# Optimization experiments

Measured on AMD Instinct MI355X. Metric: run time of the kernel, lower is better.

Reference implementation:

```python
import jax, jax.numpy as jnp
import numpy as np

N_HEAD = 12
D_MODEL = 768


def setup_inputs() -> dict:
    key = jax.random.key(0)
    ks = jax.random.split(key, 5)
    B, S, D = 8, 1024, D_MODEL
    return {
        "x": jax.random.normal(ks[0], (B, S, D), dtype=jnp.float32),
        "Wqkv": jax.random.normal(ks[1], (D, 3 * D), dtype=jnp.float32) * 0.02,
        "bqkv": jax.random.normal(ks[2], (3 * D,), dtype=jnp.float32) * 0.02,
        "Wproj": jax.random.normal(ks[3], (D, D), dtype=jnp.float32) * 0.02,
        "bproj": jax.random.normal(ks[4], (D,), dtype=jnp.float32) * 0.02,
    }


def _attention(x, Wqkv, bqkv, Wproj, bproj):
    B, S, D = x.shape
    hd = D // N_HEAD
    qkv = x @ Wqkv + bqkv                      # [B,S,3D]
    q, k, v = jnp.split(qkv, 3, axis=-1)
    # split heads -> [B,H,S,hd]
    def sh(t):
        return t.reshape(B, S, N_HEAD, hd).transpose(0, 2, 1, 3)
    q, k, v = sh(q), sh(k), sh(v)
    scores = jnp.einsum("bhqd,bhkd->bhqk", q, k) / jnp.sqrt(jnp.float32(hd))
    causal = jnp.tril(jnp.ones((S, S), dtype=bool))  # [S,S]
    mask_value = jnp.finfo(scores.dtype).min
    scores = jnp.where(causal[None, None], scores, mask_value)
    attn = jax.nn.softmax(scores, axis=-1)
    # dropout p=0.1 treated as identity (eval mode)
    out = jnp.einsum("bhqk,bhkd->bhqd", attn, v)
    out = out.transpose(0, 2, 1, 3).reshape(B, S, D)  # merge heads
    return out @ Wproj + bproj


def reference(x, Wqkv, bqkv, Wproj, bproj):
    return _attention(x, Wqkv, bqkv, Wproj, bproj)
```

## Files before the change

kernel.cpp:

```cpp
#include <hip/hip_runtime.h>
#include <cstddef>

typedef float f32x4 __attribute__((ext_vector_type(4)));
typedef short s16x4 __attribute__((ext_vector_type(4)));
typedef short s16x8 __attribute__((ext_vector_type(8)));
typedef __bf16 bf16x8 __attribute__((ext_vector_type(8)));

#define NB 8
#define NS 1024
#define ND 768
#define NH 12
#define HD 64

__device__ __forceinline__ unsigned short f2bf(float f) {
  unsigned u = __builtin_bit_cast(unsigned, f);
  u += 0x7fffu + ((u >> 16) & 1u);
  return (unsigned short)(u >> 16);
}

__device__ __forceinline__ f32x4 mfma16(bf16x8 a, bf16x8 b, f32x4 c) {
  return __builtin_amdgcn_mfma_f32_16x16x32_bf16(a, b, c, 0, 0, 0);
}

__device__ __forceinline__ bf16x8 ld8(const unsigned short* p) {
  return *reinterpret_cast<const bf16x8*>(p);
}

__device__ __forceinline__ void gload16(unsigned short* lds_dst, const unsigned short* gsrc) {
  __builtin_amdgcn_global_load_lds(
      (const __attribute__((address_space(1))) unsigned int*)gsrc,
      (__attribute__((address_space(3))) unsigned int*)lds_dst, 16, 0, 0);
}

#define VMW(N) asm volatile("s_waitcnt vmcnt(" #N ")" ::: "memory")


__global__ __launch_bounds__(256) void cvt_f32_bf16(const float* __restrict__ in,
                                                    unsigned short* __restrict__ out) {
  int i = (blockIdx.x * 256 + threadIdx.x) * 4;
  float4 v = *reinterpret_cast<const float4*>(in + i);
  ushort4 o;
  o.x = f2bf(v.x); o.y = f2bf(v.y); o.z = f2bf(v.z); o.w = f2bf(v.w);
  *reinterpret_cast<ushort4*>(out + i) = o;
}

__global__ __launch_bounds__(256) void transpose_cvt(const float* __restrict__ in,
                                                     unsigned short* __restrict__ out,
                                                     int R, int C) {
  __shared__ float tile[32][33];
  int c0 = blockIdx.x * 32, r0 = blockIdx.y * 32;
  int tx = threadIdx.x & 31, ty = threadIdx.x >> 5;
#pragma unroll
  for (int i = 0; i < 32; i += 8)
    tile[ty + i][tx] = in[(size_t)(r0 + ty + i) * C + c0 + tx];
  __syncthreads();
#pragma unroll
  for (int i = 0; i < 32; i += 8)
    out[(size_t)(c0 + ty + i) * R + r0 + tx] = f2bf(tile[tx][ty + i]);
}


#define SLOT 8192

__device__ __forceinline__ void gemm_mainloop4(const unsigned short* __restrict__ A,
                                               const unsigned short* __restrict__ Bt,
                                               int K, int m0, int n0,
                                               unsigned short* smem,
                                               f32x4 (&acc)[4][4]) {
  int tid = threadIdx.x, lane = tid & 63, wid = tid >> 6;
  int wr = wid >> 1, wc = wid & 1;
  int ll = lane & 15, lh = lane >> 4;
  int swsrc = ((lane & 3) ^ ((lane >> 3) & 3)) * 8;

  const unsigned short* asrc = A + (size_t)(m0 + wid * 32 + (lane >> 2)) * K + swsrc;
  const unsigned short* bsrc = Bt + (size_t)(n0 + wid * 32 + (lane >> 2)) * K + swsrc;
  const int sw = (lh ^ ((ll >> 1) & 3)) * 8;
  const int nt = K / 32;

  auto stage = [&](int slot, int t) {
    unsigned short* ad = smem + slot * SLOT + wid * 1024;
    unsigned short* bd = smem + slot * SLOT + 4096 + wid * 1024;
    const unsigned short* as = asrc + t * 32;
    const unsigned short* bs = bsrc + t * 32;
    gload16(ad, as);
    gload16(ad + 512, as + (size_t)16 * K);
    gload16(bd, bs);
    gload16(bd + 512, bs + (size_t)16 * K);
  };

  stage(0, 0);
  stage(1, 1);
  stage(2, 2);
  VMW(8);
  __builtin_amdgcn_s_barrier();
  asm volatile("" ::: "memory");

  for (int t = 0; t < nt; ++t) {
    if (t + 3 < nt) stage((t + 3) & 3, t + 3);

    const unsigned short* Ab = smem + (t & 3) * SLOT;
    const unsigned short* Bb = Ab + 4096;

    __builtin_amdgcn_s_setprio(1);
    bf16x8 af[4], bg[4];
#pragma unroll
    for (int m = 0; m < 4; m++) af[m] = ld8(Ab + (wr * 64 + m * 16 + ll) * 32 + sw);
#pragma unroll
    for (int n = 0; n < 4; n++) bg[n] = ld8(Bb + (wc * 64 + n * 16 + ll) * 32 + sw);
#pragma unroll
    for (int m = 0; m < 4; m++)
#pragma unroll
      for (int n = 0; n < 4; n++) acc[m][n] = mfma16(af[m], bg[n], acc[m][n]);
    __builtin_amdgcn_s_setprio(0);

    if (t + 3 < nt) {
      VMW(8);
      __builtin_amdgcn_s_barrier();
      asm volatile("" ::: "memory");
    } else if (t + 2 < nt) {
      VMW(4);
      __builtin_amdgcn_s_barrier();
      asm volatile("" ::: "memory");
    } else if (t + 1 < nt) {
      VMW(0);
      __builtin_amdgcn_s_barrier();
      asm volatile("" ::: "memory");
    }
  }
}

__device__ __forceinline__ void gemm_mainloop3(const unsigned short* __restrict__ A,
                                               const unsigned short* __restrict__ Bt,
                                               int K, int m0, int n0,
                                               unsigned short* smem,
                                               f32x4 (&acc)[4][4]) {
  int tid = threadIdx.x, lane = tid & 63, wid = tid >> 6;
  int wr = wid >> 1, wc = wid & 1;
  int ll = lane & 15, lh = lane >> 4;
  int swsrc = ((lane & 3) ^ ((lane >> 3) & 3)) * 8;

  const unsigned short* asrc = A + (size_t)(m0 + wid * 32 + (lane >> 2)) * K + swsrc;
  const unsigned short* bsrc = Bt + (size_t)(n0 + wid * 32 + (lane >> 2)) * K + swsrc;
  const int sw = (lh ^ ((ll >> 1) & 3)) * 8;
  const int nt = K / 32;

  auto stage = [&](int slot, int t) {
    unsigned short* ad = smem + slot * SLOT + wid * 1024;
    unsigned short* bd = smem + slot * SLOT + 4096 + wid * 1024;
    const unsigned short* as = asrc + t * 32;
    const unsigned short* bs = bsrc + t * 32;
    gload16(ad, as);
    gload16(ad + 512, as + (size_t)16 * K);
    gload16(bd, bs);
    gload16(bd + 512, bs + (size_t)16 * K);
  };

  stage(0, 0);
  stage(1, 1);
  VMW(4);
  __builtin_amdgcn_s_barrier();
  asm volatile("" ::: "memory");

  int slot = 0;
  for (int t = 0; t < nt; ++t) {
    if (t + 2 < nt) {
      int s2 = slot + 2; if (s2 >= 3) s2 -= 3;
      stage(s2, t + 2);
    }
    const unsigned short* Ab = smem + slot * SLOT;
    const unsigned short* Bb = Ab + 4096;

    __builtin_amdgcn_s_setprio(1);
    bf16x8 af[4], bg[4];
#pragma unroll
    for (int m = 0; m < 4; m++) af[m] = ld8(Ab + (wr * 64 + m * 16 + ll) * 32 + sw);
#pragma unroll
    for (int n = 0; n < 4; n++) bg[n] = ld8(Bb + (wc * 64 + n * 16 + ll) * 32 + sw);
#pragma unroll
    for (int m = 0; m < 4; m++)
#pragma unroll
      for (int n = 0; n < 4; n++) acc[m][n] = mfma16(af[m], bg[n], acc[m][n]);
    __builtin_amdgcn_s_setprio(0);

    if (t + 2 < nt) {
      VMW(4);
      __builtin_amdgcn_s_barrier();
      asm volatile("" ::: "memory");
    } else if (t + 2 == nt) {
      VMW(0);
      __builtin_amdgcn_s_barrier();
      asm volatile("" ::: "memory");
    }
    slot++; if (slot == 3) slot = 0;
  }
}


#define QSCALE 0.18033688f

__global__ __launch_bounds__(256, 2) void qkv_gemm(const unsigned short* __restrict__ xbf,
                                                   const unsigned short* __restrict__ WT,
                                                   const float* __restrict__ bias,
                                                   unsigned short* __restrict__ qw,
                                                   unsigned short* __restrict__ kw,
                                                   unsigned short* __restrict__ vt) {
  __shared__ __align__(16) unsigned short smem[4 * SLOT];
  int bid = blockIdx.x;
  int k8 = bid & 7, j = bid >> 3;
  int m0 = (k8 * 8 + (j & 7)) * 128;
  int n0 = (j >> 3) * 128;
  f32x4 acc[4][4];
#pragma unroll
  for (int m = 0; m < 4; m++)
#pragma unroll
    for (int n = 0; n < 4; n++) acc[m][n] = (f32x4){0.f, 0.f, 0.f, 0.f};

  gemm_mainloop4(xbf, WT, ND, m0, n0, smem, acc);

  int tid = threadIdx.x, lane = tid & 63, wid = tid >> 6;
  int wr = wid >> 1, wc = wid & 1;
  int ll = lane & 15, lh = lane >> 4;
  int which = n0 / ND;

  if (which == 2) {
#pragma unroll
    for (int nf = 0; nf < 4; nf++) {
      int col = n0 + wc * 64 + nf * 16 + ll;
      float bv = bias[col];
      int w2 = col - 2 * ND;
      int h = w2 >> 6, d = w2 & 63;
#pragma unroll
      for (int mf = 0; mf < 4; mf++) {
        int m = m0 + wr * 64 + mf * 16 + lh * 4;
        int b = m >> 10, s = m & 1023;
        s16x4 pk;
        pk[0] = (short)f2bf(acc[mf][nf][0] + bv);
        pk[1] = (short)f2bf(acc[mf][nf][1] + bv);
        pk[2] = (short)f2bf(acc[mf][nf][2] + bv);
        pk[3] = (short)f2bf(acc[mf][nf][3] + bv);
        size_t idx = (((size_t)b * NH + h) * HD + d) * NS + s;
        *(s16x4*)&vt[idx] = pk;
      }
    }
  } else {
#pragma unroll
    for (int nf = 0; nf < 4; nf++) {
      int col = n0 + wc * 64 + nf * 16 + ll;
      float bv = bias[col];
      int w2 = col - which * ND;
      int h = w2 >> 6, d = w2 & 63;
#pragma unroll
      for (int mf = 0; mf < 4; mf++) {
#pragma unroll
        for (int r = 0; r < 4; r++) {
          int m = m0 + wr * 64 + mf * 16 + lh * 4 + r;
          int b = m >> 10, s = m & 1023;
          float v = acc[mf][nf][r] + bv;
          size_t idx = (((size_t)b * NH + h) * NS + s) * HD + d;
          if (which == 0)
            qw[idx] = f2bf(v * QSCALE);
          else
            kw[idx] = f2bf(v);
        }
      }
    }
  }
}


__global__ __launch_bounds__(256, 3) void proj_gemm(const unsigned short* __restrict__ abf,
                                                    const unsigned short* __restrict__ WT,
                                                    const float* __restrict__ bias,
                                                    float* __restrict__ out) {
  __shared__ __align__(16) unsigned short smem[3 * SLOT];
  int bid = blockIdx.x;
  int k8 = bid & 7, j = bid >> 3;
  int m0 = (k8 * 8 + (j & 7)) * 128;
  int n0 = (j >> 3) * 128;
  f32x4 acc[4][4];
#pragma unroll
  for (int m = 0; m < 4; m++)
#pragma unroll
    for (int n = 0; n < 4; n++) acc[m][n] = (f32x4){0.f, 0.f, 0.f, 0.f};

  gemm_mainloop3(abf, WT, ND, m0, n0, smem, acc);

  int tid = threadIdx.x, lane = tid & 63, wid = tid >> 6;
  int wr = wid >> 1, wc = wid & 1;
  int ll = lane & 15, lh = lane >> 4;
#pragma unroll
  for (int nf = 0; nf < 4; nf++) {
    int col = n0 + wc * 64 + nf * 16 + ll;
    float bv = bias[col];
#pragma unroll
    for (int mf = 0; mf < 4; mf++) {
#pragma unroll
      for (int r = 0; r < 4; r++) {
        int m = m0 + wr * 64 + mf * 16 + lh * 4 + r;
        out[(size_t)m * ND + col] = acc[mf][nf][r] + bv;
      }
    }
  }
}


#define LP 88
#define KVSLOT 8192

__global__ __launch_bounds__(512) void attn_kernel(const unsigned short* __restrict__ qw,
                                                   const unsigned short* __restrict__ kw,
                                                   const unsigned short* __restrict__ vt,
                                                   unsigned short* __restrict__ attn_out) {
  int bid = blockIdx.x;
  int xcd = bid & 7, j = bid >> 3;
  int grp = xcd * 12 + (j % 12);
  int qt = 7 - (j / 12);
  int b = grp / NH, h = grp % NH;
  __shared__ __align__(16) unsigned short KV[3 * KVSLOT];
  __shared__ __align__(16) unsigned short Ps[8][16 * LP];

  int tid = threadIdx.x, lane = tid & 63, wid = tid >> 6;
  int ll = lane & 15, lh = lane >> 4, r7x = ll & 7;
  int q0 = qt * 128, q0w = q0 + wid * 16;
  const size_t bhk = ((size_t)b * NH + h) * NS * HD;
  const size_t bhv = ((size_t)b * NH + h) * HD * NS;

  bf16x8 qf0 = ld8(&qw[bhk + (size_t)(q0w + ll) * HD + lh * 8]);
  bf16x8 qf1 = ld8(&qw[bhk + (size_t)(q0w + ll) * HD + 32 + lh * 8]);

  f32x4 o[4];
#pragma unroll
  for (int n = 0; n < 4; n++) o[n] = (f32x4){0.f, 0.f, 0.f, 0.f};
  float m_r = -1e30f, l_r = 0.f;

  int srow = tid >> 3;
  int scol = ((tid & 7) ^ ((tid >> 3) & 7)) * 8;
  const unsigned short* ksrc = kw + bhk + (size_t)srow * HD + scol;
  const unsigned short* vsrc = vt + bhv + (size_t)srow * NS + scol;

  unsigned short* pw = &Ps[wid][ll * LP];
  const int qme = q0w + ll;
  const int qmaxw = q0w + 15;
  const int nt = 2 * (qt + 1);

  auto stage = [&](int slot, int t) {
    unsigned short* kd = KV + slot * KVSLOT + wid * 512;
    unsigned short* vd = KV + slot * KVSLOT + 4096 + wid * 512;
    gload16(kd, ksrc + (size_t)t * 64 * HD);
    gload16(vd, vsrc + t * 64);
  };

  stage(0, 0);
  stage(1, 1);
  VMW(2);
  __builtin_amdgcn_s_barrier();
  asm volatile("" ::: "memory");

  int slot = 0;
  for (int t = 0; t < nt; ++t) {
    if (t + 2 < nt) {
      int s2 = slot + 2; if (s2 >= 3) s2 -= 3;
      stage(s2, t + 2);
    }
    int j0 = t * 64;

    if (j0 <= qmaxw) {
      const unsigned short* Kb = KV + slot * KVSLOT;
      const unsigned short* Vb = Kb + 4096;

      f32x4 sa[4];
#pragma unroll
      for (int n = 0; n < 4; n++) {
        bf16x8 kf0 = ld8(Kb + (n * 16 + ll) * 64 + (lh ^ r7x) * 8);
        bf16x8 kf1 = ld8(Kb + (n * 16 + ll) * 64 + ((4 + lh) ^ r7x) * 8);
        sa[n] = mfma16(kf0, qf0, (f32x4){0.f, 0.f, 0.f, 0.f});
        sa[n] = mfma16(kf1, qf1, sa[n]);
      }

      if (j0 + 63 > q0w) {
#pragma unroll
        for (int n = 0; n < 4; n++)
#pragma unroll
          for (int r = 0; r < 4; r++)
            if (j0 + n * 16 + lh * 4 + r > qme) sa[n][r] = -1e30f;
      }

      float t0 = fmaxf(fmaxf(sa[0][0], sa[0][1]), fmaxf(sa[0][2], sa[0][3]));
      float t1 = fmaxf(fmaxf(sa[1][0], sa[1][1]), fmaxf(sa[1][2], sa[1][3]));
      float t2 = fmaxf(fmaxf(sa[2][0], sa[2][1]), fmaxf(sa[2][2], sa[2][3]));
      float t3 = fmaxf(fmaxf(sa[3][0], sa[3][1]), fmaxf(sa[3][2], sa[3][3]));
      float tmax = fmaxf(fmaxf(t0, t1), fmaxf(t2, t3));
      tmax = fmaxf(tmax, __shfl_xor(tmax, 16));
      tmax = fmaxf(tmax, __shfl_xor(tmax, 32));

      if (!__all(tmax - m_r <= 11.5f)) {
        float mnew = fmaxf(m_r, tmax);
        float alpha = exp2f(m_r - mnew);
        m_r = mnew;
        l_r *= alpha;
        float ab0 = __shfl(alpha, lh * 4 + 0);
        float ab1 = __shfl(alpha, lh * 4 + 1);
        float ab2 = __shfl(alpha, lh * 4 + 2);
        float ab3 = __shfl(alpha, lh * 4 + 3);
#pragma unroll
        for (int n2 = 0; n2 < 4; n2++) {
          o[n2][0] *= ab0; o[n2][1] *= ab1; o[n2][2] *= ab2; o[n2][3] *= ab3;
        }
      }

      float p[4][4];
      float ssum = 0.f;
#pragma unroll
      for (int n = 0; n < 4; n++)
#pragma unroll
        for (int r = 0; r < 4; r++) {
          p[n][r] = exp2f(sa[n][r] - m_r);
          ssum += p[n][r];
        }
      ssum += __shfl_xor(ssum, 16);
      ssum += __shfl_xor(ssum, 32);
      l_r += ssum;

#pragma unroll
      for (int n = 0; n < 4; n++) {
        s16x4 pk;
        pk[0] = (short)f2bf(p[n][0]);
        pk[1] = (short)f2bf(p[n][1]);
        pk[2] = (short)f2bf(p[n][2]);
        pk[3] = (short)f2bf(p[n][3]);
        *(s16x4*)&pw[n * 16 + lh * 4] = pk;
      }

#pragma unroll
      for (int c = 0; c < 2; c++) {
        bf16x8 pf = ld8(&pw[c * 32 + lh * 8]);
#pragma unroll
        for (int n2 = 0; n2 < 4; n2++) {
          bf16x8 vf = ld8(Vb + (n2 * 16 + ll) * 64 + ((c * 4 + lh) ^ r7x) * 8);
          o[n2] = mfma16(pf, vf, o[n2]);
        }
      }
    }

    if (t + 2 < nt) {
      VMW(2);
      __builtin_amdgcn_s_barrier();
      asm volatile("" ::: "memory");
    } else if (t + 2 == nt) {
      VMW(0);
      __builtin_amdgcn_s_barrier();
      asm volatile("" ::: "memory");
    }
    slot++; if (slot == 3) slot = 0;
  }

  float lrec = 1.0f / l_r;
  float lb0 = __shfl(lrec, lh * 4 + 0);
  float lb1 = __shfl(lrec, lh * 4 + 1);
  float lb2 = __shfl(lrec, lh * 4 + 2);
  float lb3 = __shfl(lrec, lh * 4 + 3);
#pragma unroll
  for (int n2 = 0; n2 < 4; n2++) {
    int d = n2 * 16 + ll;
    int qb = q0w + lh * 4;
    attn_out[((size_t)b * NS + qb + 0) * ND + h * HD + d] = f2bf(o[n2][0] * lb0);
    attn_out[((size_t)b * NS + qb + 1) * ND + h * HD + d] = f2bf(o[n2][1] * lb1);
    attn_out[((size_t)b * NS + qb + 2) * ND + h * HD + d] = f2bf(o[n2][2] * lb2);
    attn_out[((size_t)b * NS + qb + 3) * ND + h * HD + d] = f2bf(o[n2][3] * lb3);
  }
}


extern "C" void kernel_launch(void* const* d_in, const int* in_sizes, int n_in,
                              void* d_out, int out_size, void* d_ws, size_t ws_size,
                              hipStream_t stream) {
  const float* x = (const float*)d_in[0];
  const float* Wqkv = (const float*)d_in[1];
  const float* bqkv = (const float*)d_in[2];
  const float* Wproj = (const float*)d_in[3];
  const float* bproj = (const float*)d_in[4];
  float* out = (float*)d_out;

  char* ws = (char*)d_ws;
  const size_t SZ_X = (size_t)NB * NS * ND * 2;
  const size_t SZ_WQKV = (size_t)ND * 3 * ND * 2;
  const size_t SZ_WPROJ = (size_t)ND * ND * 2;
  const size_t SZ_HEAD = (size_t)NB * NH * NS * HD;

  unsigned short* xbf = (unsigned short*)(ws);
  unsigned short* wqkvT = (unsigned short*)(ws + SZ_X);
  unsigned short* wprojT = (unsigned short*)(ws + SZ_X + SZ_WQKV);
  unsigned short* qw = (unsigned short*)(ws + SZ_X + SZ_WQKV + SZ_WPROJ);
  unsigned short* kw = qw + SZ_HEAD;
  unsigned short* vt = kw + SZ_HEAD;
  unsigned short* attn = vt + SZ_HEAD;

  (void)in_sizes; (void)n_in; (void)out_size; (void)ws_size;

  cvt_f32_bf16<<<(NB * NS * ND) / 1024, 256, 0, stream>>>(x, xbf);
  transpose_cvt<<<dim3(3 * ND / 32, ND / 32), 256, 0, stream>>>(Wqkv, wqkvT, ND, 3 * ND);
  transpose_cvt<<<dim3(ND / 32, ND / 32), 256, 0, stream>>>(Wproj, wprojT, ND, ND);

  qkv_gemm<<<1152, 256, 0, stream>>>(xbf, wqkvT, bqkv, qw, kw, vt);

  attn_kernel<<<768, 512, 0, stream>>>(qw, kw, vt, attn);

  proj_gemm<<<384, 256, 0, stream>>>(attn, wprojT, bproj, out);
}
```

Measured before the change: 115.2 us.

## Enlarge QKV GEMM tile to 256x128 with three-stage pipeline

The QKV projection GEMM now uses a 256x128 output tile per block (each wave computes 128x64), which halves the grid and doubles reuse of each B fragment loaded from LDS. The four-slot, depth-3 prefetch is replaced by a three-slot, depth-2 pipeline with larger slots, keeping LDS use bounded. The aim is to cut global and LDS traffic per MFMA. In exchange, register pressure rises from 64 to 128 accumulator floats per lane, which may hurt occupancy under launch_bounds(256,2). With 576 blocks, wave-quantisation over the CUs also changes.

```diff
diff --git a/kernel.cpp b/kernel.cpp
--- a/kernel.cpp
+++ b/kernel.cpp
@@ -60,9 +60,76 @@
 }
 
 
+#define SLOT_Q 12288
 #define SLOT 8192
 
-__device__ __forceinline__ void gemm_mainloop4(const unsigned short* __restrict__ A,
+__device__ __forceinline__ void gemm_mainloop_q(const unsigned short* __restrict__ A,
+                                                const unsigned short* __restrict__ Bt,
+                                                int K, int m0, int n0,
+                                                unsigned short* smem,
+                                                f32x4 (&acc)[8][4]) {
+  int tid = threadIdx.x, lane = tid & 63, wid = tid >> 6;
+  int wr = wid >> 1, wc = wid & 1;
+  int ll = lane & 15, lh = lane >> 4;
+  int swsrc = ((lane & 3) ^ ((lane >> 3) & 3)) * 8;
+
+  const unsigned short* asrc = A + (size_t)(m0 + wid * 64 + (lane >> 2)) * K + swsrc;
+  const unsigned short* bsrc = Bt + (size_t)(n0 + wid * 32 + (lane >> 2)) * K + swsrc;
+  const int sw = (lh ^ ((ll >> 1) & 3)) * 8;
+  const int nt = K / 32;
+
+  auto stage = [&](int slot, int t) {
+    unsigned short* ad = smem + slot * SLOT_Q + wid * 2048;
+    unsigned short* bd = smem + slot * SLOT_Q + 8192 + wid * 1024;
+    const unsigned short* as = asrc + t * 32;
+    const unsigned short* bs = bsrc + t * 32;
+#pragma unroll
+    for (int i = 0; i < 4; i++) gload16(ad + i * 512, as + (size_t)i * 16 * K);
+#pragma unroll
+    for (int i = 0; i < 2; i++) gload16(bd + i * 512, bs + (size_t)i * 16 * K);
+  };
+
+  stage(0, 0);
+  stage(1, 1);
+  VMW(6);
+  __builtin_amdgcn_s_barrier();
+  asm volatile("" ::: "memory");
+
+  int slot = 0;
+  for (int t = 0; t < nt; ++t) {
+    if (t + 2 < nt) {
+      int s2 = slot + 2; if (s2 >= 3) s2 -= 3;
+      stage(s2, t + 2);
+    }
+    const unsigned short* Ab = smem + slot * SLOT_Q;
+    const unsigned short* Bb = Ab + 8192;
+
+    __builtin_amdgcn_s_setprio(1);
+    bf16x8 af[8], bg[4];
+#pragma unroll
+    for (int m = 0; m < 8; m++) af[m] = ld8(Ab + (wr * 128 + m * 16 + ll) * 32 + sw);
+#pragma unroll
+    for (int n = 0; n < 4; n++) bg[n] = ld8(Bb + (wc * 64 + n * 16 + ll) * 32 + sw);
+#pragma unroll
+    for (int m = 0; m < 8; m++)
+#pragma unroll
+      for (int n = 0; n < 4; n++) acc[m][n] = mfma16(af[m], bg[n], acc[m][n]);
+    __builtin_amdgcn_s_setprio(0);
+
+    if (t + 2 < nt) {
+      VMW(6);
+      __builtin_amdgcn_s_barrier();
+      asm volatile("" ::: "memory");
+    } else if (t + 2 == nt) {
+      VMW(0);
+      __builtin_amdgcn_s_barrier();
+      asm volatile("" ::: "memory");
+    }
+    slot++; if (slot == 3) slot = 0;
+  }
+}
+
+__device__ __forceinline__ void gemm_mainloop3(const unsigned short* __restrict__ A,
                                                const unsigned short* __restrict__ Bt,
                                                int K, int m0, int n0,
                                                unsigned short* smem,
@@ -90,73 +157,6 @@
 
   stage(0, 0);
   stage(1, 1);
-  stage(2, 2);
-  VMW(8);
-  __builtin_amdgcn_s_barrier();
-  asm volatile("" ::: "memory");
-
-  for (int t = 0; t < nt; ++t) {
-    if (t + 3 < nt) stage((t + 3) & 3, t + 3);
-
-    const unsigned short* Ab = smem + (t & 3) * SLOT;
-    const unsigned short* Bb = Ab + 4096;
-
-    __builtin_amdgcn_s_setprio(1);
-    bf16x8 af[4], bg[4];
-#pragma unroll
-    for (int m = 0; m < 4; m++) af[m] = ld8(Ab + (wr * 64 + m * 16 + ll) * 32 + sw);
-#pragma unroll
-    for (int n = 0; n < 4; n++) bg[n] = ld8(Bb + (wc * 64 + n * 16 + ll) * 32 + sw);
-#pragma unroll
-    for (int m = 0; m < 4; m++)
-#pragma unroll
-      for (int n = 0; n < 4; n++) acc[m][n] = mfma16(af[m], bg[n], acc[m][n]);
-    __builtin_amdgcn_s_setprio(0);
-
-    if (t + 3 < nt) {
-      VMW(8);
-      __builtin_amdgcn_s_barrier();
-      asm volatile("" ::: "memory");
-    } else if (t + 2 < nt) {
-      VMW(4);
-      __builtin_amdgcn_s_barrier();
-      asm volatile("" ::: "memory");
-    } else if (t + 1 < nt) {
-      VMW(0);
-      __builtin_amdgcn_s_barrier();
-      asm volatile("" ::: "memory");
-    }
-  }
-}
-
-__device__ __forceinline__ void gemm_mainloop3(const unsigned short* __restrict__ A,
-                                               const unsigned short* __restrict__ Bt,
-                                               int K, int m0, int n0,
-                                               unsigned short* smem,
-                                               f32x4 (&acc)[4][4]) {
-  int tid = threadIdx.x, lane = tid & 63, wid = tid >> 6;
-  int wr = wid >> 1, wc = wid & 1;
-  int ll = lane & 15, lh = lane >> 4;
-  int swsrc = ((lane & 3) ^ ((lane >> 3) & 3)) * 8;
-
-  const unsigned short* asrc = A + (size_t)(m0 + wid * 32 + (lane >> 2)) * K + swsrc;
-  const unsigned short* bsrc = Bt + (size_t)(n0 + wid * 32 + (lane >> 2)) * K + swsrc;
-  const int sw = (lh ^ ((ll >> 1) & 3)) * 8;
-  const int nt = K / 32;
-
-  auto stage = [&](int slot, int t) {
-    unsigned short* ad = smem + slot * SLOT + wid * 1024;
-    unsigned short* bd = smem + slot * SLOT + 4096 + wid * 1024;
-    const unsigned short* as = asrc + t * 32;
-    const unsigned short* bs = bsrc + t * 32;
-    gload16(ad, as);
-    gload16(ad + 512, as + (size_t)16 * K);
-    gload16(bd, bs);
-    gload16(bd + 512, bs + (size_t)16 * K);
-  };
-
-  stage(0, 0);
-  stage(1, 1);
   VMW(4);
   __builtin_amdgcn_s_barrier();
   asm volatile("" ::: "memory");
@@ -204,18 +204,18 @@
                                                    unsigned short* __restrict__ qw,
                                                    unsigned short* __restrict__ kw,
                                                    unsigned short* __restrict__ vt) {
-  __shared__ __align__(16) unsigned short smem[4 * SLOT];
+  __shared__ __align__(16) unsigned short smem[3 * SLOT_Q];
   int bid = blockIdx.x;
   int k8 = bid & 7, j = bid >> 3;
-  int m0 = (k8 * 8 + (j & 7)) * 128;
-  int n0 = (j >> 3) * 128;
-  f32x4 acc[4][4];
-#pragma unroll
-  for (int m = 0; m < 4; m++)
+  int m0 = (k8 * 4 + (j & 3)) * 256;
+  int n0 = (j >> 2) * 128;
+  f32x4 acc[8][4];
+#pragma unroll
+  for (int m = 0; m < 8; m++)
 #pragma unroll
     for (int n = 0; n < 4; n++) acc[m][n] = (f32x4){0.f, 0.f, 0.f, 0.f};
 
-  gemm_mainloop4(xbf, WT, ND, m0, n0, smem, acc);
+  gemm_mainloop_q(xbf, WT, ND, m0, n0, smem, acc);
 
   int tid = threadIdx.x, lane = tid & 63, wid = tid >> 6;
   int wr = wid >> 1, wc = wid & 1;
@@ -230,8 +230,8 @@
       int w2 = col - 2 * ND;
       int h = w2 >> 6, d = w2 & 63;
 #pragma unroll
-      for (int mf = 0; mf < 4; mf++) {
-        int m = m0 + wr * 64 + mf * 16 + lh * 4;
+      for (int mf = 0; mf < 8; mf++) {
+        int m = m0 + wr * 128 + mf * 16 + lh * 4;
         int b = m >> 10, s = m & 1023;
         s16x4 pk;
         pk[0] = (short)f2bf(acc[mf][nf][0] + bv);
@@ -250,10 +250,10 @@
       int w2 = col - which * ND;
       int h = w2 >> 6, d = w2 & 63;
 #pragma unroll
-      for (int mf = 0; mf < 4; mf++) {
+      for (int mf = 0; mf < 8; mf++) {
 #pragma unroll
         for (int r = 0; r < 4; r++) {
-          int m = m0 + wr * 64 + mf * 16 + lh * 4 + r;
+          int m = m0 + wr * 128 + mf * 16 + lh * 4 + r;
           int b = m >> 10, s = m & 1023;
           float v = acc[mf][nf][r] + bv;
           size_t idx = (((size_t)b * NH + h) * NS + s) * HD + d;
@@ -501,7 +501,7 @@
   transpose_cvt<<<dim3(3 * ND / 32, ND / 32), 256, 0, stream>>>(Wqkv, wqkvT, ND, 3 * ND);
   transpose_cvt<<<dim3(ND / 32, ND / 32), 256, 0, stream>>>(Wproj, wprojT, ND, ND);
 
-  qkv_gemm<<<1152, 256, 0, stream>>>(xbf, wqkvT, bqkv, qw, kw, vt);
+  qkv_gemm<<<576, 256, 0, stream>>>(xbf, wqkvT, bqkv, qw, kw, vt);
 
   attn_kernel<<<768, 512, 0, stream>>>(qw, kw, vt, attn);
 
```

Result: slower. 120.1 us (+4.3%).

## Double attention query tile per block to reuse staged K/V tiles

Applied to the files above, without the earlier changes.

Each attention block now processes 256 queries (two 16-row groups per wave) instead of 128, halving the grid to 384 blocks. Each K/V tile staged into LDS is reused by twice as many queries, cutting global K/V loads and staging barriers. The trade-off is fewer blocks for the CU count, worse causal load imbalance, and higher register pressure from doubled accumulators.

```diff
diff --git a/kernel.cpp b/kernel.cpp
--- a/kernel.cpp
+++ b/kernel.cpp
@@ -314,24 +314,30 @@
   int bid = blockIdx.x;
   int xcd = bid & 7, j = bid >> 3;
   int grp = xcd * 12 + (j % 12);
-  int qt = 7 - (j / 12);
+  int qt = 3 - (j / 12);
   int b = grp / NH, h = grp % NH;
   __shared__ __align__(16) unsigned short KV[3 * KVSLOT];
   __shared__ __align__(16) unsigned short Ps[8][16 * LP];
 
   int tid = threadIdx.x, lane = tid & 63, wid = tid >> 6;
   int ll = lane & 15, lh = lane >> 4, r7x = ll & 7;
-  int q0 = qt * 128, q0w = q0 + wid * 16;
+  int q0 = qt * 256, q0w = q0 + wid * 32;
   const size_t bhk = ((size_t)b * NH + h) * NS * HD;
   const size_t bhv = ((size_t)b * NH + h) * HD * NS;
 
-  bf16x8 qf0 = ld8(&qw[bhk + (size_t)(q0w + ll) * HD + lh * 8]);
-  bf16x8 qf1 = ld8(&qw[bhk + (size_t)(q0w + ll) * HD + 32 + lh * 8]);
-
-  f32x4 o[4];
-#pragma unroll
-  for (int n = 0; n < 4; n++) o[n] = (f32x4){0.f, 0.f, 0.f, 0.f};
-  float m_r = -1e30f, l_r = 0.f;
+  bf16x8 qf[2][2];
+#pragma unroll
+  for (int g = 0; g < 2; g++) {
+    qf[g][0] = ld8(&qw[bhk + (size_t)(q0w + g * 16 + ll) * HD + lh * 8]);
+    qf[g][1] = ld8(&qw[bhk + (size_t)(q0w + g * 16 + ll) * HD + 32 + lh * 8]);
+  }
+
+  f32x4 o[2][4];
+#pragma unroll
+  for (int g = 0; g < 2; g++)
+#pragma unroll
+    for (int n = 0; n < 4; n++) o[g][n] = (f32x4){0.f, 0.f, 0.f, 0.f};
+  float m_r[2] = {-1e30f, -1e30f}, l_r[2] = {0.f, 0.f};
 
   int srow = tid >> 3;
   int scol = ((tid & 7) ^ ((tid >> 3) & 7)) * 8;
@@ -339,9 +345,8 @@
   const unsigned short* vsrc = vt + bhv + (size_t)srow * NS + scol;
 
   unsigned short* pw = &Ps[wid][ll * LP];
-  const int qme = q0w + ll;
-  const int qmaxw = q0w + 15;
-  const int nt = 2 * (qt + 1);
+  const int qmaxw = q0w + 31;
+  const int nt = 4 * (qt + 1);
 
   auto stage = [&](int slot, int t) {
     unsigned short* kd = KV + slot * KVSLOT + wid * 512;
@@ -368,78 +373,84 @@
       const unsigned short* Kb = KV + slot * KVSLOT;
       const unsigned short* Vb = Kb + 4096;
 
-      f32x4 sa[4];
-#pragma unroll
-      for (int n = 0; n < 4; n++) {
-        bf16x8 kf0 = ld8(Kb + (n * 16 + ll) * 64 + (lh ^ r7x) * 8);
-        bf16x8 kf1 = ld8(Kb + (n * 16 + ll) * 64 + ((4 + lh) ^ r7x) * 8);
-        sa[n] = mfma16(kf0, qf0, (f32x4){0.f, 0.f, 0.f, 0.f});
-        sa[n] = mfma16(kf1, qf1, sa[n]);
-      }
-
-      if (j0 + 63 > q0w) {
+#pragma unroll
+      for (int g = 0; g < 2; g++) {
+        f32x4 sa[4];
+#pragma unroll
+        for (int n = 0; n < 4; n++) {
+          bf16x8 kf0 = ld8(Kb + (n * 16 + ll) * 64 + (lh ^ r7x) * 8);
+          bf16x8 kf1 = ld8(Kb + (n * 16 + ll) * 64 + ((4 + lh) ^ r7x) * 8);
+          sa[n] = mfma16(kf0, qf[g][0], (f32x4){0.f, 0.f, 0.f, 0.f});
+          sa[n] = mfma16(kf1, qf[g][1], sa[n]);
+        }
+
+        int qbase = q0w + g * 16;
+        if (j0 + 63 > qbase) {
+          int qme = qbase + ll;
+#pragma unroll
+          for (int n = 0; n < 4; n++)
+#pragma unroll
+            for (int r = 0; r < 4; r++)
+              if (j0 + n * 16 + lh * 4 + r > qme) sa[n][r] = -1e30f;
+        }
+
+        float t0 = fmaxf(fmaxf(sa[0][0], sa[0][1]), fmaxf(sa[0][2], sa[0][3]));
+        float t1 = fmaxf(fmaxf(sa[1][0], sa[1][1]), fmaxf(sa[1][2], sa[1][3]));
+        float t2 = fmaxf(fmaxf(sa[2][0], sa[2][1]), fmaxf(sa[2][2], sa[2][3]));
+        float t3 = fmaxf(fmaxf(sa[3][0], sa[3][1]), fmaxf(sa[3][2], sa[3][3]));
+        float tmax = fmaxf(fmaxf(t0, t1), fmaxf(t2, t3));
+        tmax = fmaxf(tmax, __shfl_xor(tmax, 16));
+        tmax = fmaxf(tmax, __shfl_xor(tmax, 32));
+
+        if (!__all(tmax - m_r[g] <= 11.5f)) {
+          float mnew = fmaxf(m_r[g], tmax);
+          float alpha = exp2f(m_r[g] - mnew);
+          m_r[g] = mnew;
+          l_r[g] *= alpha;
+          float ab0 = __shfl(alpha, lh * 4 + 0);
+          float ab1 = __shfl(alpha, lh * 4 + 1);
+          float ab2 = __shfl(alpha, lh * 4 + 2);
+          float ab3 = __shfl(alpha, lh * 4 + 3);
+#pragma unroll
+          for (int n2 = 0; n2 < 4; n2++) {
+            o[g][n2][0] *= ab0; o[g][n2][1] *= ab1;
+            o[g][n2][2] *= ab2; o[g][n2][3] *= ab3;
+          }
+        }
+
+        float p[4][4];
+        float ssum = 0.f;
 #pragma unroll
         for (int n = 0; n < 4; n++)
 #pragma unroll
-          for (int r = 0; r < 4; r++)
-            if (j0 + n * 16 + lh * 4 + r > qme) sa[n][r] = -1e30f;
-      }
-
-      float t0 = fmaxf(fmaxf(sa[0][0], sa[0][1]), fmaxf(sa[0][2], sa[0][3]));
-      float t1 = fmaxf(fmaxf(sa[1][0], sa[1][1]), fmaxf(sa[1][2], sa[1][3]));
-      float t2 = fmaxf(fmaxf(sa[2][0], sa[2][1]), fmaxf(sa[2][2], sa[2][3]));
-      float t3 = fmaxf(fmaxf(sa[3][0], sa[3][1]), fmaxf(sa[3][2], sa[3][3]));
-      float tmax = fmaxf(fmaxf(t0, t1), fmaxf(t2, t3));
-      tmax = fmaxf(tmax, __shfl_xor(tmax, 16));
-      tmax = fmaxf(tmax, __shfl_xor(tmax, 32));
-
-      if (!__all(tmax - m_r <= 11.5f)) {
-        float mnew = fmaxf(m_r, tmax);
-        float alpha = exp2f(m_r - mnew);
-        m_r = mnew;
-        l_r *= alpha;
-        float ab0 = __shfl(alpha, lh * 4 + 0);
-        float ab1 = __shfl(alpha, lh * 4 + 1);
-        float ab2 = __shfl(alpha, lh * 4 + 2);
-        float ab3 = __shfl(alpha, lh * 4 + 3);
-#pragma unroll
-        for (int n2 = 0; n2 < 4; n2++) {
-          o[n2][0] *= ab0; o[n2][1] *= ab1; o[n2][2] *= ab2; o[n2][3] *= ab3;
+          for (int r = 0; r < 4; r++) {
+            p[n][r] = exp2f(sa[n][r] - m_r[g]);
+            ssum += p[n][r];
+          }
+        ssum += __shfl_xor(ssum, 16);
+        ssum += __shfl_xor(ssum, 32);
+        l_r[g] += ssum;
+
+#pragma unroll
+        for (int n = 0; n < 4; n++) {
+          s16x4 pk;
+          pk[0] = (short)f2bf(p[n][0]);
+          pk[1] = (short)f2bf(p[n][1]);
+          pk[2] = (short)f2bf(p[n][2]);
+          pk[3] = (short)f2bf(p[n][3]);
+          *(s16x4*)&pw[n * 16 + lh * 4] = pk;
+        }
+
+#pragma unroll
+        for (int c = 0; c < 2; c++) {
+          bf16x8 pf = ld8(&pw[c * 32 + lh * 8]);
+#pragma unroll
+          for (int n2 = 0; n2 < 4; n2++) {
+            bf16x8 vf = ld8(Vb + (n2 * 16 + ll) * 64 + ((c * 4 + lh) ^ r7x) * 8);
+            o[g][n2] = mfma16(pf, vf, o[g][n2]);
+          }
         }
       }
-
-      float p[4][4];
-      float ssum = 0.f;
-#pragma unroll
-      for (int n = 0; n < 4; n++)
-#pragma unroll
-        for (int r = 0; r < 4; r++) {
-          p[n][r] = exp2f(sa[n][r] - m_r);
-          ssum += p[n][r];
-        }
-      ssum += __shfl_xor(ssum, 16);
-      ssum += __shfl_xor(ssum, 32);
-      l_r += ssum;
-
-#pragma unroll
-      for (int n = 0; n < 4; n++) {
-        s16x4 pk;
-        pk[0] = (short)f2bf(p[n][0]);
-        pk[1] = (short)f2bf(p[n][1]);
-        pk[2] = (short)f2bf(p[n][2]);
-        pk[3] = (short)f2bf(p[n][3]);
-        *(s16x4*)&pw[n * 16 + lh * 4] = pk;
-      }
-
-#pragma unroll
-      for (int c = 0; c < 2; c++) {
-        bf16x8 pf = ld8(&pw[c * 32 + lh * 8]);
-#pragma unroll
-        for (int n2 = 0; n2 < 4; n2++) {
-          bf16x8 vf = ld8(Vb + (n2 * 16 + ll) * 64 + ((c * 4 + lh) ^ r7x) * 8);
-          o[n2] = mfma16(pf, vf, o[n2]);
-        }
-      }
     }
 
     if (t + 2 < nt) {
@@ -454,19 +465,22 @@
     slot++; if (slot == 3) slot = 0;
   }
 
-  float lrec = 1.0f / l_r;
-  float lb0 = __shfl(lrec, lh * 4 + 0);
-  float lb1 = __shfl(lrec, lh * 4 + 1);
-  float lb2 = __shfl(lrec, lh * 4 + 2);
-  float lb3 = __shfl(lrec, lh * 4 + 3);
-#pragma unroll
-  for (int n2 = 0; n2 < 4; n2++) {
-    int d = n2 * 16 + ll;
-    int qb = q0w + lh * 4;
-    attn_out[((size_t)b * NS + qb + 0) * ND + h * HD + d] = f2bf(o[n2][0] * lb0);
-    attn_out[((size_t)b * NS + qb + 1) * ND + h * HD + d] = f2bf(o[n2][1] * lb1);
-    attn_out[((size_t)b * NS + qb + 2) * ND + h * HD + d] = f2bf(o[n2][2] * lb2);
-    attn_out[((size_t)b * NS + qb + 3) * ND + h * HD + d] = f2bf(o[n2][3] * lb3);
+#pragma unroll
+  for (int g = 0; g < 2; g++) {
+    float lrec = 1.0f / l_r[g];
+    float lb0 = __shfl(lrec, lh * 4 + 0);
+    float lb1 = __shfl(lrec, lh * 4 + 1);
+    float lb2 = __shfl(lrec, lh * 4 + 2);
+    float lb3 = __shfl(lrec, lh * 4 + 3);
+#pragma unroll
+    for (int n2 = 0; n2 < 4; n2++) {
+      int d = n2 * 16 + ll;
+      int qb = q0w + g * 16 + lh * 4;
+      attn_out[((size_t)b * NS + qb + 0) * ND + h * HD + d] = f2bf(o[g][n2][0] * lb0);
+      attn_out[((size_t)b * NS + qb + 1) * ND + h * HD + d] = f2bf(o[g][n2][1] * lb1);
+      attn_out[((size_t)b * NS + qb + 2) * ND + h * HD + d] = f2bf(o[g][n2][2] * lb2);
+      attn_out[((size_t)b * NS + qb + 3) * ND + h * HD + d] = f2bf(o[g][n2][3] * lb3);
+    }
   }
 }
 
@@ -503,7 +517,7 @@
 
   qkv_gemm<<<1152, 256, 0, stream>>>(xbf, wqkvT, bqkv, qw, kw, vt);
 
-  attn_kernel<<<768, 512, 0, stream>>>(qw, kw, vt, attn);
+  attn_kernel<<<384, 512, 0, stream>>>(qw, kw, vt, attn);
 
   proj_gemm<<<384, 256, 0, stream>>>(attn, wprojT, bproj, out);
 }
```

New measurement: 122.8 us. 1.07x slower.
